# Kernel optimization log

Measured on AMD Instinct MI355X. Metric: run time of the kernel, lower is better.

## Reference

```python
import jax, jax.numpy as jnp
import numpy as np

L = 3          # num_modification_layers
MOD_SCALE = 0.01


def setup_inputs() -> dict:
    key = jax.random.key(0)
    B, E = 8192, 1024
    ks = jax.random.split(key, 12)
    sg = 1.0 / np.sqrt(E)        # GRUCell / Linear(E,.) init bound
    sh = 1.0 / np.sqrt(E // 2)   # Linear(E//2, E) init bound
    u = lambda k, shape, s: jax.random.uniform(k, shape, jnp.float32, -s, s)
    return {
        "x":    jax.random.normal(ks[0], (B, E), jnp.float32),
        # GRUCell params (PyTorch layout: gates ordered r, z, n)
        "W_ih": u(ks[1], (L, 3 * E, E), sg),
        "W_hh": u(ks[2], (L, 3 * E, E), sg),
        "b_ih": u(ks[3], (L, 3 * E), sg),
        "b_hh": u(ks[4], (L, 3 * E), sg),
        # modification network: Linear(E, E//2) -> ReLU -> Linear(E//2, E) -> Tanh
        "W1":   u(ks[5], (L, E // 2, E), sg),
        "b1":   u(ks[6], (L, E // 2), sg),
        "W2":   u(ks[7], (L, E, E // 2), sh),
        "b2":   u(ks[8], (L, E), sh),
        # modification gate: Linear(E, 1) -> Sigmoid
        "Wg":   u(ks[9], (L, 1, E), sg),
        "bg":   u(ks[10], (L, 1), sg),
    }


def reference(x, W_ih, W_hh, b_ih, b_hh, W1, b1, W2, b2, Wg, bg):
    B, E = x.shape
    h_prev = jnp.zeros((B, E), x.dtype)  # hidden states reset to zeros
    cur = x
    for l in range(L):
        # modification network (small MLP) + scalar gate
        sig = jnp.tanh(jax.nn.relu(cur @ W1[l].T + b1[l]) @ W2[l].T + b2[l])  # (B, E)
        gate = jax.nn.sigmoid(cur @ Wg[l].T + bg[l])                           # (B, 1)
        cond = jnp.mean(gate) > 0.5
        # data-dependent self-modification: weight_ih += scale * mean(sig)[None,:]
        # (row-broadcast over the 3E gate rows), predicated on-device
        wih = jnp.where(cond,
                        W_ih[l] + MOD_SCALE * jnp.mean(sig, axis=0)[None, :],
                        W_ih[l])
        # GRUCell (PyTorch semantics)
        gi = cur @ wih.T + b_ih[l]            # (B, 3E)
        gh = h_prev @ W_hh[l].T + b_hh[l]     # (B, 3E) -- h_prev is zeros
        i_r, i_z, i_n = jnp.split(gi, 3, axis=1)
        h_r, h_z, h_n = jnp.split(gh, 3, axis=1)
        r = jax.nn.sigmoid(i_r + h_r)
        z = jax.nn.sigmoid(i_z + h_z)
        n = jnp.tanh(i_n + r * h_n)
        h = (1.0 - z) * n + z * h_prev
        cur = h + sig
    return cur
```

## Files before the change

### kernel.cpp

```cpp
#include <hip/hip_runtime.h>
#include <cstdint>
#include <cstddef>


#define BSZ 8192
#define ESZ 1024

typedef _Float16 f16x8 __attribute__((ext_vector_type(8)));
typedef float    f32x4 __attribute__((ext_vector_type(4)));
typedef unsigned short u16;
typedef u16 u16x4 __attribute__((ext_vector_type(4)));

__device__ __forceinline__ u16 f2h(float f) {
    _Float16 h = (_Float16)f;
    return __builtin_bit_cast(u16, h);
}
__device__ __forceinline__ float h2f(u16 h) {
    return (float)__builtin_bit_cast(_Float16, h);
}

__device__ __forceinline__ void gload16(const void* g, void* l) {
    __builtin_amdgcn_global_load_lds((const __attribute__((address_space(1))) void*)g,
                                     (__attribute__((address_space(3))) void*)l,
                                     16, 0, 0);
}

__device__ __forceinline__ int swzi(int row, int chunk) {
    return (row << 6) + (((chunk ^ row) & 7) << 3);
}

__device__ __forceinline__ float sigmoidf_(float x) {
    return 1.f / (1.f + __expf(-x));
}
__device__ __forceinline__ float tanhf_(float x) {
    float cx = fminf(fmaxf(x, -15.f), 15.f);
    float e = __expf(2.f * cx);
    return (e - 1.f) / (e + 1.f);
}

#define N4_WIH (3 * 3072 * 1024 / 4)
#define N4_W1  (3 * 512 * 1024 / 4)
#define N4_W2  (3 * 1024 * 512 / 4)
#define N4_X   (BSZ * ESZ / 4)

__global__ void cvt_all_kernel(const float* __restrict__ Wih, const float* __restrict__ W1,
                               const float* __restrict__ W2, const float* __restrict__ x,
                               u16* __restrict__ oWih, u16* __restrict__ oW1,
                               u16* __restrict__ oW2, u16* __restrict__ ox) {
    int i = blockIdx.x * 256 + threadIdx.x;
    const float* in;
    u16* out;
    if (i < N4_WIH) { in = Wih; out = oWih; }
    else if (i < N4_WIH + N4_W1) { i -= N4_WIH; in = W1; out = oW1; }
    else if (i < N4_WIH + N4_W1 + N4_W2) { i -= N4_WIH + N4_W1; in = W2; out = oW2; }
    else { i -= N4_WIH + N4_W1 + N4_W2; if (i >= N4_X) return; in = x; out = ox; }
    f32x4 v = ((const f32x4*)in)[i];
    u16x4 o;
    o.x = f2h(v.x); o.y = f2h(v.y); o.z = f2h(v.z); o.w = f2h(v.w);
    ((u16x4*)out)[i] = o;
}

__global__ void gate_kernel(const u16* __restrict__ cur, const float* __restrict__ Wg,
                            const float* __restrict__ bg, const float* __restrict__ colsum,
                            float* __restrict__ gsum, float* __restrict__ sdot) {
    const int wid = threadIdx.x >> 6, lane = threadIdx.x & 63;
    const int row = blockIdx.x * 4 + wid;
    const u16* cr = cur + (size_t)row * ESZ;
    float pg = 0.f, pm = 0.f;
#pragma unroll
    for (int h = 0; h < 2; h++) {
        int base = lane * 16 + h * 8;
        f16x8 cv = *(const f16x8*)(cr + base);
#pragma unroll
        for (int q = 0; q < 2; q++) {
            f32x4 wv = *(const f32x4*)(Wg + base + q * 4);
            f32x4 mv = *(const f32x4*)(colsum + base + q * 4);
#pragma unroll
            for (int e = 0; e < 4; e++) {
                float c = (float)cv[q * 4 + e];
                pg += c * wv[e];
                pm += c * mv[e];
            }
        }
    }
#pragma unroll
    for (int s = 32; s >= 1; s >>= 1) {
        pg += __shfl_xor(pg, s);
        pm += __shfl_xor(pm, s);
    }
    __shared__ float gp[4];
    if (lane == 0) {
        gp[wid] = sigmoidf_(pg + bg[0]);
        sdot[row] = pm * (0.01f / 8192.f);
    }
    __syncthreads();
    if (threadIdx.x == 0) atomicAdd(gsum, gp[0] + gp[1] + gp[2] + gp[3]);
}

template <int ACT>
__global__ void __launch_bounds__(256, 3) gemm_act_kernel(
    const u16* __restrict__ A, const u16* __restrict__ W,
    const float* __restrict__ bias, u16* __restrict__ outp,
    float* __restrict__ colsum, int N, int K, int nshift) {
    __shared__ u16 lA[2][128 * 64];
    __shared__ u16 lB[2][64 * 64];
    const int t = threadIdx.x;
    const int chunk = gridDim.x >> 3;
    const int o = blockIdx.x;
    const int tl = (o & 7) * chunk + (o >> 3);
    const int m0 = (tl >> nshift) * 128;
    const int n0 = (tl & ((1 << nshift) - 1)) * 64;
    const int wid = t >> 6, lane = t & 63;
    const int waver = wid >> 1, wavec = wid & 1;
    const int lrow = lane & 15, lk = lane >> 4;

    f32x4 acc[4][2] = {};

    auto STAGE = [&](int buf, int k0) {
#pragma unroll
        for (int i = 0; i < 4; i++) {
            int eo = i * 2048 + t * 8;
            int r = eo >> 6;
            int gc = (((eo >> 3) ^ r) & 7) << 3;
            gload16(A + (size_t)(m0 + r) * K + k0 + gc, &lA[buf][eo]);
        }
#pragma unroll
        for (int i = 0; i < 2; i++) {
            int eo = i * 2048 + t * 8;
            int r = eo >> 6;
            int gc = (((eo >> 3) ^ r) & 7) << 3;
            gload16(W + (size_t)(n0 + r) * K + k0 + gc, &lB[buf][eo]);
        }
    };

    STAGE(0, 0);
    const int nk = K >> 6;
    int cur = 0;
    for (int kt = 0; kt < nk; ++kt) {
        __syncthreads();
        if (kt + 1 < nk) STAGE(cur ^ 1, (kt + 1) * 64);
#pragma unroll
        for (int kk = 0; kk < 2; kk++) {
            f16x8 af[4], bf[2];
#pragma unroll
            for (int m = 0; m < 4; m++)
                af[m] = *(const f16x8*)&lA[cur][swzi(waver * 64 + m * 16 + lrow, kk * 4 + lk)];
#pragma unroll
            for (int n = 0; n < 2; n++)
                bf[n] = *(const f16x8*)&lB[cur][swzi(wavec * 32 + n * 16 + lrow, kk * 4 + lk)];
#pragma unroll
            for (int m = 0; m < 4; m++)
#pragma unroll
                for (int n = 0; n < 2; n++)
                    acc[m][n] = __builtin_amdgcn_mfma_f32_16x16x32_f16(af[m], bf[n], acc[m][n], 0, 0, 0);
        }
        cur ^= 1;
    }

#pragma unroll
    for (int n = 0; n < 2; n++) {
        int c = n0 + wavec * 32 + n * 16 + lrow;
        float bv = bias[c];
        float cs = 0.f;
#pragma unroll
        for (int m = 0; m < 4; m++) {
            int rbase = m0 + waver * 64 + m * 16 + lk * 4;
#pragma unroll
            for (int j = 0; j < 4; j++) {
                float v = acc[m][n][j] + bv;
                if (ACT == 0) {
                    v = v > 0.f ? v : 0.f;
                    outp[(size_t)(rbase + j) * N + c] = f2h(v);
                } else {
                    float tv = tanhf_(v);
                    outp[(size_t)(rbase + j) * N + c] = f2h(tv);
                    cs += tv;
                }
            }
        }
        if (ACT == 1) {
            cs += __shfl_xor(cs, 16);
            cs += __shfl_xor(cs, 32);
            if (lane < 16) atomicAdd(&colsum[c], cs);
        }
    }
}

__global__ void __launch_bounds__(256, 2) gemm_gru_kernel(
    const u16* __restrict__ Ab, const u16* __restrict__ Wb,
    const float* __restrict__ bih, const float* __restrict__ bhh,
    const u16* __restrict__ sig, const float* __restrict__ sdot,
    const float* __restrict__ gsum, float* __restrict__ curf_out,
    u16* __restrict__ curb_out) {
    __shared__ u16 lA[2][128 * 64];
    __shared__ u16 lB[2][3][64 * 64];
    const int t = threadIdx.x;
    const int hw = blockIdx.y * 16 + blockIdx.x;
    const int xcd = hw & 7, idx = hw >> 3;
    const int m0 = (idx >> 1) * 128, c0 = ((xcd << 1) | (idx & 1)) * 64;
    const int wid = t >> 6, lane = t & 63;
    const int waver = wid >> 1, wavec = wid & 1;
    const int lrow = lane & 15, lk = lane >> 4;
    const int K = ESZ, E = ESZ;

    const int eoA = t * 8;
    f32x4 acc[4][6] = {};

    auto STAGE = [&](int buf, int k0) {
#pragma unroll
        for (int i = 0; i < 4; i++) {
            int eo = i * 2048 + eoA;
            int r = eo >> 6;
            int gc = (((eo >> 3) ^ r) & 7) << 3;
            gload16(Ab + (size_t)(m0 + r) * K + k0 + gc, &lA[buf][eo]);
        }
#pragma unroll
        for (int g = 0; g < 3; g++)
#pragma unroll
            for (int i = 0; i < 2; i++) {
                int eo = i * 2048 + eoA;
                int r = eo >> 6;
                int gc = (((eo >> 3) ^ r) & 7) << 3;
                gload16(Wb + (size_t)(g * 1024 + c0 + r) * K + k0 + gc, &lB[buf][g][eo]);
            }
    };

    STAGE(0, 0);
    int cur = 0;
    for (int kt = 0; kt < 16; ++kt) {
        __syncthreads();
        if (kt < 15) STAGE(cur ^ 1, (kt + 1) * 64);
#pragma unroll
        for (int kk = 0; kk < 2; kk++) {
            f16x8 af[4];
#pragma unroll
            for (int m = 0; m < 4; m++)
                af[m] = *(const f16x8*)&lA[cur][swzi(waver * 64 + m * 16 + lrow, kk * 4 + lk)];
#pragma unroll
            for (int g = 0; g < 3; g++) {
#pragma unroll
                for (int n = 0; n < 2; n++) {
                    f16x8 bf = *(const f16x8*)&lB[cur][g][swzi(wavec * 32 + n * 16 + lrow, kk * 4 + lk)];
#pragma unroll
                    for (int m = 0; m < 4; m++)
                        acc[m][g * 2 + n] =
                            __builtin_amdgcn_mfma_f32_16x16x32_f16(af[m], bf, acc[m][g * 2 + n], 0, 0, 0);
                }
            }
        }
        cur ^= 1;
    }

    const bool cond = (*gsum) > 4096.f;
#pragma unroll
    for (int m = 0; m < 4; m++) {
        int rbase = m0 + waver * 64 + m * 16 + lk * 4;
        float corr[4];
#pragma unroll
        for (int j = 0; j < 4; j++) corr[j] = cond ? sdot[rbase + j] : 0.f;
#pragma unroll
        for (int n = 0; n < 2; n++) {
            int c = c0 + wavec * 32 + n * 16 + lrow;
            float br = bih[c], bz = bih[E + c], bn = bih[2 * E + c];
            float hr = bhh[c], hz = bhh[E + c], hn = bhh[2 * E + c];
#pragma unroll
            for (int j = 0; j < 4; j++) {
                float ir = acc[m][0 + n][j] + br + corr[j];
                float iz = acc[m][2 + n][j] + bz + corr[j];
                float inn = acc[m][4 + n][j] + bn + corr[j];
                float r = sigmoidf_(ir + hr);
                float z = sigmoidf_(iz + hz);
                float nn = tanhf_(inn + r * hn);
                float h = (1.f - z) * nn;
                float o = h + h2f(sig[(size_t)(rbase + j) * E + c]);
                if (curf_out) curf_out[(size_t)(rbase + j) * E + c] = o;
                if (curb_out) curb_out[(size_t)(rbase + j) * E + c] = f2h(o);
            }
        }
    }
}

extern "C" void kernel_launch(void* const* d_in, const int* in_sizes, int n_in,
                              void* d_out, int out_size, void* d_ws, size_t ws_size,
                              hipStream_t stream) {
    const float* x   = (const float*)d_in[0];
    const float* Wih = (const float*)d_in[1];
    const float* bih = (const float*)d_in[3];
    const float* bhh = (const float*)d_in[4];
    const float* W1  = (const float*)d_in[5];
    const float* b1  = (const float*)d_in[6];
    const float* W2  = (const float*)d_in[7];
    const float* b2  = (const float*)d_in[8];
    const float* Wg  = (const float*)d_in[9];
    const float* bg  = (const float*)d_in[10];
    float* out = (float*)d_out;

    char* w = (char*)d_ws;
    u16* Wihb  = (u16*)w;  w += (size_t)3 * 3072 * 1024 * 2;
    u16* W1b   = (u16*)w;  w += (size_t)3 * 512 * 1024 * 2;
    u16* W2b   = (u16*)w;  w += (size_t)3 * 1024 * 512 * 2;
    u16* curbA = (u16*)w;  w += (size_t)BSZ * ESZ * 2;
    u16* curbB = (u16*)w;  w += (size_t)BSZ * ESZ * 2;
    u16* Amat  = (u16*)w;  w += (size_t)BSZ * 512 * 2;
    u16* sigb  = (u16*)w;  w += (size_t)BSZ * ESZ * 2;
    float* colsum = (float*)w;  w += 4096;
    float* gsum   = (float*)w;  w += 256;
    float* sdot   = (float*)w;  w += (size_t)BSZ * 4;

    {
        int n4 = N4_WIH + N4_W1 + N4_W2 + N4_X;
        cvt_all_kernel<<<dim3((n4 + 255) / 256), 256, 0, stream>>>(
            Wih, W1, W2, x, Wihb, W1b, W2b, curbA);
    }

    u16* cin = curbA;
    u16* cout = curbB;
    for (int l = 0; l < 3; l++) {
        hipMemsetAsync(colsum, 0, 4096 + 4, stream);
        gemm_act_kernel<0><<<dim3(512), 256, 0, stream>>>(
            cin, W1b + (size_t)l * 512 * 1024, b1 + l * 512, Amat, nullptr, 512, 1024, 3);
        gemm_act_kernel<1><<<dim3(1024), 256, 0, stream>>>(
            Amat, W2b + (size_t)l * 1024 * 512, b2 + l * 1024, sigb, colsum, 1024, 512, 4);
        gate_kernel<<<dim3(BSZ / 4), 256, 0, stream>>>(
            cin, Wg + l * 1024, bg + l, colsum, gsum, sdot);
        gemm_gru_kernel<<<dim3(16, BSZ / 128), 256, 0, stream>>>(
            cin, Wihb + (size_t)l * 3072 * 1024, bih + l * 3072, bhh + l * 3072,
            sigb, sdot, gsum, (l == 2) ? out : nullptr, (l < 2) ? cout : nullptr);
        u16* tmp = cin; cin = cout; cout = tmp;
    }
}
```

Baseline: 582.3 us.

## Fuse W1 and W_ih GEMMs into one wide kernel, split GRU epilogue

Both the first modification-network GEMM and the GRU input GEMM read the same activation, so they are merged into one kernel. It uses 512 threads, 256-row tiles and 4 column groups per block, so the A tile is loaded once for both. The GRU pre-activations are written to an fp16 buffer of size B x 3E, and a separate elementwise kernel applies the gate correction, sigmoid/tanh and residual. The second GEMM also moves to larger 256x128 tiles. In exchange the code adds an extra 48MB write and read per layer for the gi buffer, rounds gi to fp16 before the nonlinearities, and uses bigger tiles that may reduce occupancy.

```diff
diff --git a/kernel.cpp b/kernel.cpp
--- a/kernel.cpp
+++ b/kernel.cpp
@@ -97,132 +97,41 @@
     if (threadIdx.x == 0) atomicAdd(gsum, gp[0] + gp[1] + gp[2] + gp[3]);
 }
 
-template <int ACT>
-__global__ void __launch_bounds__(256, 3) gemm_act_kernel(
-    const u16* __restrict__ A, const u16* __restrict__ W,
-    const float* __restrict__ bias, u16* __restrict__ outp,
-    float* __restrict__ colsum, int N, int K, int nshift) {
-    __shared__ u16 lA[2][128 * 64];
-    __shared__ u16 lB[2][64 * 64];
+__global__ void __launch_bounds__(512, 2) gemm_big_kernel(
+    const u16* __restrict__ A, const u16* __restrict__ W1l, const u16* __restrict__ Wihl,
+    const float* __restrict__ b1l, const float* __restrict__ bihl,
+    u16* __restrict__ Amat, u16* __restrict__ gi) {
+    __shared__ u16 lA[2][256 * 64];
+    __shared__ u16 lB[2][4][64 * 64];
     const int t = threadIdx.x;
-    const int chunk = gridDim.x >> 3;
-    const int o = blockIdx.x;
-    const int tl = (o & 7) * chunk + (o >> 3);
-    const int m0 = (tl >> nshift) * 128;
-    const int n0 = (tl & ((1 << nshift) - 1)) * 64;
+    const int xcd = blockIdx.x & 7, q = blockIdx.x >> 3;
+    const int m0 = (xcd * 4 + (q & 3)) * 256;
+    const int cb = q >> 2;
     const int wid = t >> 6, lane = t & 63;
     const int waver = wid >> 1, wavec = wid & 1;
     const int lrow = lane & 15, lk = lane >> 4;
-
-    f32x4 acc[4][2] = {};
+    const int K = 1024;
+
+    f32x4 acc[4][8] = {};
 
     auto STAGE = [&](int buf, int k0) {
 #pragma unroll
         for (int i = 0; i < 4; i++) {
-            int eo = i * 2048 + t * 8;
+            int eo = i * 4096 + t * 8;
             int r = eo >> 6;
             int gc = (((eo >> 3) ^ r) & 7) << 3;
             gload16(A + (size_t)(m0 + r) * K + k0 + gc, &lA[buf][eo]);
         }
 #pragma unroll
-        for (int i = 0; i < 2; i++) {
-            int eo = i * 2048 + t * 8;
+        for (int g = 0; g < 4; g++) {
+            int cg = cb * 4 + g;
+            const u16* Wp = (cg < 8) ? (W1l + (size_t)cg * 64 * K)
+                                     : (Wihl + (size_t)(cg - 8) * 64 * K);
+            int eo = t * 8;
             int r = eo >> 6;
             int gc = (((eo >> 3) ^ r) & 7) << 3;
-            gload16(W + (size_t)(n0 + r) * K + k0 + gc, &lB[buf][eo]);
-        }
-    };
-
-    STAGE(0, 0);
-    const int nk = K >> 6;
-    int cur = 0;
-    for (int kt = 0; kt < nk; ++kt) {
-        __syncthreads();
-        if (kt + 1 < nk) STAGE(cur ^ 1, (kt + 1) * 64);
-#pragma unroll
-        for (int kk = 0; kk < 2; kk++) {
-            f16x8 af[4], bf[2];
-#pragma unroll
-            for (int m = 0; m < 4; m++)
-                af[m] = *(const f16x8*)&lA[cur][swzi(waver * 64 + m * 16 + lrow, kk * 4 + lk)];
-#pragma unroll
-            for (int n = 0; n < 2; n++)
-                bf[n] = *(const f16x8*)&lB[cur][swzi(wavec * 32 + n * 16 + lrow, kk * 4 + lk)];
-#pragma unroll
-            for (int m = 0; m < 4; m++)
-#pragma unroll
-                for (int n = 0; n < 2; n++)
-                    acc[m][n] = __builtin_amdgcn_mfma_f32_16x16x32_f16(af[m], bf[n], acc[m][n], 0, 0, 0);
-        }
-        cur ^= 1;
-    }
-
-#pragma unroll
-    for (int n = 0; n < 2; n++) {
-        int c = n0 + wavec * 32 + n * 16 + lrow;
-        float bv = bias[c];
-        float cs = 0.f;
-#pragma unroll
-        for (int m = 0; m < 4; m++) {
-            int rbase = m0 + waver * 64 + m * 16 + lk * 4;
-#pragma unroll
-            for (int j = 0; j < 4; j++) {
-                float v = acc[m][n][j] + bv;
-                if (ACT == 0) {
-                    v = v > 0.f ? v : 0.f;
-                    outp[(size_t)(rbase + j) * N + c] = f2h(v);
-                } else {
-                    float tv = tanhf_(v);
-                    outp[(size_t)(rbase + j) * N + c] = f2h(tv);
-                    cs += tv;
-                }
-            }
-        }
-        if (ACT == 1) {
-            cs += __shfl_xor(cs, 16);
-            cs += __shfl_xor(cs, 32);
-            if (lane < 16) atomicAdd(&colsum[c], cs);
-        }
-    }
-}
-
-__global__ void __launch_bounds__(256, 2) gemm_gru_kernel(
-    const u16* __restrict__ Ab, const u16* __restrict__ Wb,
-    const float* __restrict__ bih, const float* __restrict__ bhh,
-    const u16* __restrict__ sig, const float* __restrict__ sdot,
-    const float* __restrict__ gsum, float* __restrict__ curf_out,
-    u16* __restrict__ curb_out) {
-    __shared__ u16 lA[2][128 * 64];
-    __shared__ u16 lB[2][3][64 * 64];
-    const int t = threadIdx.x;
-    const int hw = blockIdx.y * 16 + blockIdx.x;
-    const int xcd = hw & 7, idx = hw >> 3;
-    const int m0 = (idx >> 1) * 128, c0 = ((xcd << 1) | (idx & 1)) * 64;
-    const int wid = t >> 6, lane = t & 63;
-    const int waver = wid >> 1, wavec = wid & 1;
-    const int lrow = lane & 15, lk = lane >> 4;
-    const int K = ESZ, E = ESZ;
-
-    const int eoA = t * 8;
-    f32x4 acc[4][6] = {};
-
-    auto STAGE = [&](int buf, int k0) {
-#pragma unroll
-        for (int i = 0; i < 4; i++) {
-            int eo = i * 2048 + eoA;
-            int r = eo >> 6;
-            int gc = (((eo >> 3) ^ r) & 7) << 3;
-            gload16(Ab + (size_t)(m0 + r) * K + k0 + gc, &lA[buf][eo]);
-        }
-#pragma unroll
-        for (int g = 0; g < 3; g++)
-#pragma unroll
-            for (int i = 0; i < 2; i++) {
-                int eo = i * 2048 + eoA;
-                int r = eo >> 6;
-                int gc = (((eo >> 3) ^ r) & 7) << 3;
-                gload16(Wb + (size_t)(g * 1024 + c0 + r) * K + k0 + gc, &lB[buf][g][eo]);
-            }
+            gload16(Wp + (size_t)r * K + k0 + gc, &lB[buf][g][eo]);
+        }
     };
 
     STAGE(0, 0);
@@ -237,7 +146,7 @@
             for (int m = 0; m < 4; m++)
                 af[m] = *(const f16x8*)&lA[cur][swzi(waver * 64 + m * 16 + lrow, kk * 4 + lk)];
 #pragma unroll
-            for (int g = 0; g < 3; g++) {
+            for (int g = 0; g < 4; g++) {
 #pragma unroll
                 for (int n = 0; n < 2; n++) {
                     f16x8 bf = *(const f16x8*)&lB[cur][g][swzi(wavec * 32 + n * 16 + lrow, kk * 4 + lk)];
@@ -251,32 +160,155 @@
         cur ^= 1;
     }
 
-    const bool cond = (*gsum) > 4096.f;
-#pragma unroll
-    for (int m = 0; m < 4; m++) {
-        int rbase = m0 + waver * 64 + m * 16 + lk * 4;
-        float corr[4];
-#pragma unroll
-        for (int j = 0; j < 4; j++) corr[j] = cond ? sdot[rbase + j] : 0.f;
+#pragma unroll
+    for (int g = 0; g < 4; g++) {
+        int cg = cb * 4 + g;
 #pragma unroll
         for (int n = 0; n < 2; n++) {
-            int c = c0 + wavec * 32 + n * 16 + lrow;
-            float br = bih[c], bz = bih[E + c], bn = bih[2 * E + c];
-            float hr = bhh[c], hz = bhh[E + c], hn = bhh[2 * E + c];
-#pragma unroll
-            for (int j = 0; j < 4; j++) {
-                float ir = acc[m][0 + n][j] + br + corr[j];
-                float iz = acc[m][2 + n][j] + bz + corr[j];
-                float inn = acc[m][4 + n][j] + bn + corr[j];
-                float r = sigmoidf_(ir + hr);
-                float z = sigmoidf_(iz + hz);
-                float nn = tanhf_(inn + r * hn);
-                float h = (1.f - z) * nn;
-                float o = h + h2f(sig[(size_t)(rbase + j) * E + c]);
-                if (curf_out) curf_out[(size_t)(rbase + j) * E + c] = o;
-                if (curb_out) curb_out[(size_t)(rbase + j) * E + c] = f2h(o);
-            }
-        }
+            int cl = wavec * 32 + n * 16 + lrow;
+            if (cg < 8) {
+                int c = cg * 64 + cl;
+                float bv = b1l[c];
+#pragma unroll
+                for (int m = 0; m < 4; m++) {
+                    int rbase = m0 + waver * 64 + m * 16 + lk * 4;
+#pragma unroll
+                    for (int j = 0; j < 4; j++) {
+                        float v = acc[m][g * 2 + n][j] + bv;
+                        Amat[(size_t)(rbase + j) * 512 + c] = f2h(v > 0.f ? v : 0.f);
+                    }
+                }
+            } else {
+                int c = (cg - 8) * 64 + cl;
+                float bv = bihl[c];
+#pragma unroll
+                for (int m = 0; m < 4; m++) {
+                    int rbase = m0 + waver * 64 + m * 16 + lk * 4;
+#pragma unroll
+                    for (int j = 0; j < 4; j++)
+                        gi[(size_t)(rbase + j) * 3072 + c] = f2h(acc[m][g * 2 + n][j] + bv);
+                }
+            }
+        }
+    }
+}
+
+__global__ void __launch_bounds__(512, 2) gemm_act1_kernel(
+    const u16* __restrict__ A, const u16* __restrict__ W,
+    const float* __restrict__ bias, u16* __restrict__ outp,
+    float* __restrict__ colsum) {
+    __shared__ u16 lA[2][256 * 64];
+    __shared__ u16 lB[2][2][64 * 64];
+    const int t = threadIdx.x;
+    const int xcd = blockIdx.x & 7, q = blockIdx.x >> 3;
+    const int m0 = (xcd * 4 + (q & 3)) * 256;
+    const int c0 = (q >> 2) * 128;
+    const int wid = t >> 6, lane = t & 63;
+    const int waver = wid >> 1, wavec = wid & 1;
+    const int lrow = lane & 15, lk = lane >> 4;
+    const int K = 512;
+
+    f32x4 acc[4][4] = {};
+
+    auto STAGE = [&](int buf, int k0) {
+#pragma unroll
+        for (int i = 0; i < 4; i++) {
+            int eo = i * 4096 + t * 8;
+            int r = eo >> 6;
+            int gc = (((eo >> 3) ^ r) & 7) << 3;
+            gload16(A + (size_t)(m0 + r) * K + k0 + gc, &lA[buf][eo]);
+        }
+#pragma unroll
+        for (int g = 0; g < 2; g++) {
+            int eo = t * 8;
+            int r = eo >> 6;
+            int gc = (((eo >> 3) ^ r) & 7) << 3;
+            gload16(W + (size_t)(c0 + g * 64 + r) * K + k0 + gc, &lB[buf][g][eo]);
+        }
+    };
+
+    STAGE(0, 0);
+    int cur = 0;
+    for (int kt = 0; kt < 8; ++kt) {
+        __syncthreads();
+        if (kt < 7) STAGE(cur ^ 1, (kt + 1) * 64);
+#pragma unroll
+        for (int kk = 0; kk < 2; kk++) {
+            f16x8 af[4];
+#pragma unroll
+            for (int m = 0; m < 4; m++)
+                af[m] = *(const f16x8*)&lA[cur][swzi(waver * 64 + m * 16 + lrow, kk * 4 + lk)];
+#pragma unroll
+            for (int g = 0; g < 2; g++) {
+#pragma unroll
+                for (int n = 0; n < 2; n++) {
+                    f16x8 bf = *(const f16x8*)&lB[cur][g][swzi(wavec * 32 + n * 16 + lrow, kk * 4 + lk)];
+#pragma unroll
+                    for (int m = 0; m < 4; m++)
+                        acc[m][g * 2 + n] =
+                            __builtin_amdgcn_mfma_f32_16x16x32_f16(af[m], bf, acc[m][g * 2 + n], 0, 0, 0);
+                }
+            }
+        }
+        cur ^= 1;
+    }
+
+#pragma unroll
+    for (int g = 0; g < 2; g++) {
+#pragma unroll
+        for (int n = 0; n < 2; n++) {
+            int c = c0 + g * 64 + wavec * 32 + n * 16 + lrow;
+            float bv = bias[c];
+            float cs = 0.f;
+#pragma unroll
+            for (int m = 0; m < 4; m++) {
+                int rbase = m0 + waver * 64 + m * 16 + lk * 4;
+#pragma unroll
+                for (int j = 0; j < 4; j++) {
+                    float tv = tanhf_(acc[m][g * 2 + n][j] + bv);
+                    outp[(size_t)(rbase + j) * 1024 + c] = f2h(tv);
+                    cs += tv;
+                }
+            }
+            cs += __shfl_xor(cs, 16);
+            cs += __shfl_xor(cs, 32);
+            if (lane < 16) atomicAdd(&colsum[c], cs);
+        }
+    }
+}
+
+__global__ void gru_finish_kernel(const u16* __restrict__ gi, const u16* __restrict__ sig,
+                                  const float* __restrict__ bhh, const float* __restrict__ sdot,
+                                  const float* __restrict__ gsum, float* __restrict__ curf,
+                                  u16* __restrict__ curb) {
+    const int i = blockIdx.x * 256 + threadIdx.x;
+    const int row = i >> 7;
+    const int cc = (i & 127) * 8;
+    const u16* gr = gi + (size_t)row * 3072;
+    f16x8 vr = *(const f16x8*)(gr + cc);
+    f16x8 vz = *(const f16x8*)(gr + 1024 + cc);
+    f16x8 vn = *(const f16x8*)(gr + 2048 + cc);
+    f16x8 vs = *(const f16x8*)(sig + (size_t)row * 1024 + cc);
+    const float corr = (*gsum > 4096.f) ? sdot[row] : 0.f;
+    float o[8];
+#pragma unroll
+    for (int j = 0; j < 8; j++) {
+        float hr = bhh[cc + j], hz = bhh[1024 + cc + j], hn = bhh[2048 + cc + j];
+        float r = sigmoidf_((float)vr[j] + corr + hr);
+        float z = sigmoidf_((float)vz[j] + corr + hz);
+        float n = tanhf_((float)vn[j] + corr + r * hn);
+        o[j] = (1.f - z) * n + (float)vs[j];
+    }
+    if (curb) {
+        f16x8 ov;
+#pragma unroll
+        for (int j = 0; j < 8; j++) ov[j] = (_Float16)o[j];
+        *(f16x8*)(curb + (size_t)row * 1024 + cc) = ov;
+    }
+    if (curf) {
+        float* dst = curf + (size_t)row * 1024 + cc;
+#pragma unroll
+        for (int j = 0; j < 8; j++) dst[j] = o[j];
     }
 }
 
@@ -303,6 +335,7 @@
     u16* curbB = (u16*)w;  w += (size_t)BSZ * ESZ * 2;
     u16* Amat  = (u16*)w;  w += (size_t)BSZ * 512 * 2;
     u16* sigb  = (u16*)w;  w += (size_t)BSZ * ESZ * 2;
+    u16* gib   = (u16*)w;  w += (size_t)BSZ * 3072 * 2;
     float* colsum = (float*)w;  w += 4096;
     float* gsum   = (float*)w;  w += 256;
     float* sdot   = (float*)w;  w += (size_t)BSZ * 4;
@@ -317,15 +350,16 @@
     u16* cout = curbB;
     for (int l = 0; l < 3; l++) {
         hipMemsetAsync(colsum, 0, 4096 + 4, stream);
-        gemm_act_kernel<0><<<dim3(512), 256, 0, stream>>>(
-            cin, W1b + (size_t)l * 512 * 1024, b1 + l * 512, Amat, nullptr, 512, 1024, 3);
-        gemm_act_kernel<1><<<dim3(1024), 256, 0, stream>>>(
-            Amat, W2b + (size_t)l * 1024 * 512, b2 + l * 1024, sigb, colsum, 1024, 512, 4);
+        gemm_big_kernel<<<dim3(448), 512, 0, stream>>>(
+            cin, W1b + (size_t)l * 512 * 1024, Wihb + (size_t)l * 3072 * 1024,
+            b1 + l * 512, bih + l * 3072, Amat, gib);
+        gemm_act1_kernel<<<dim3(256), 512, 0, stream>>>(
+            Amat, W2b + (size_t)l * 1024 * 512, b2 + l * 1024, sigb, colsum);
         gate_kernel<<<dim3(BSZ / 4), 256, 0, stream>>>(
             cin, Wg + l * 1024, bg + l, colsum, gsum, sdot);
-        gemm_gru_kernel<<<dim3(16, BSZ / 128), 256, 0, stream>>>(
-            cin, Wihb + (size_t)l * 3072 * 1024, bih + l * 3072, bhh + l * 3072,
-            sigb, sdot, gsum, (l == 2) ? out : nullptr, (l < 2) ? cout : nullptr);
+        gru_finish_kernel<<<dim3(BSZ * ESZ / 8 / 256), 256, 0, stream>>>(
+            gib, sigb, bhh + l * 3072, sdot, gsum,
+            (l == 2) ? out : nullptr, (l < 2) ? cout : nullptr);
         u16* tmp = cin; cin = cout; cout = tmp;
     }
 }
```

Measured after the change: 598.2 us. +2.7%, slower.
